# Kernel tuning notes

Hardware: AMD Instinct MI355X
Metric: run time of the kernel (lower is better)

Reference implementation:

```python
import jax, jax.numpy as jnp
import numpy as np

N = 65536
R = 9          # num_relations + 1
D_IN = 256
D_HID = 512
D_OUT = 256
N_HIDDEN = 2


def _xavier(key, shape):
    fan_out, fan_in = shape[-2], shape[-1]
    limit = np.sqrt(6.0 / (fan_in + fan_out))
    return jax.random.uniform(key, shape, jnp.float32, -limit, limit)


def setup_inputs() -> dict:
    key = jax.random.key(0)
    ks = jax.random.split(key, 12)
    inp = {
        "x": jax.random.normal(ks[0], (N, D_IN), jnp.float32),
        "edge_attr": jax.random.uniform(ks[1], (N, R), jnp.float32),
    }
    dims = [(D_HID, D_IN)] + [(D_HID, D_HID)] * N_HIDDEN + [(D_OUT, D_HID)]
    for i, (o, ii) in enumerate(dims):
        inp[f"W{i}"] = _xavier(ks[2 + 2 * i], (R, o, ii))
        inp[f"b{i}"] = _xavier(ks[3 + 2 * i], (R, o))
    return inp


def _linear_kg(x, edge_attr, W, b):
    # roi,ni,nr->no : relation-mixed linear per node
    y = jnp.einsum("roi,ni,nr->no", W, x, edge_attr)
    return y + edge_attr @ b


def reference(x, edge_attr, W0, b0, W1, b1, W2, b2, W3, b3):
    y = jax.nn.relu(_linear_kg(x, edge_attr, W0, b0))
    y = jax.nn.relu(_linear_kg(y, edge_attr, W1, b1))
    y = jax.nn.relu(_linear_kg(y, edge_attr, W2, b2))
    y = _linear_kg(y, edge_attr, W3, b3)
    return y
```

## Files before the change

### kernel.cpp

```cpp
#include <hip/hip_runtime.h>
#include <stdint.h>

using f32x4  = __attribute__((ext_vector_type(4))) float;
using bf16x8 = __attribute__((ext_vector_type(8))) __bf16;

#define GLOAD_LDS16(src, dst) __builtin_amdgcn_global_load_lds(                 \
    (const __attribute__((address_space(1))) void*)(src),                      \
    (__attribute__((address_space(3))) void*)(dst), 16, 0, 0)


__global__ void cvt_x_kernel(const float* __restrict__ x, __bf16* __restrict__ out) {
    const int u    = blockIdx.x * 256 + threadIdx.x;
    const int lane = u & 63;
    const int f    = (u >> 6) & 31;
    const int c    = (u >> 11) & 1;
    const int rb   = u >> 12;
    const int row  = rb * 128 + ((f >> 2) << 4) + (lane & 15);
    const int i    = c * 128 + ((f & 3) << 5) + ((lane >> 4) << 3);
    const float4 a = *(const float4*)(x + (size_t)row * 256 + i);
    const float4 b = *(const float4*)(x + (size_t)row * 256 + i + 4);
    bf16x8 pv;
    pv[0] = (__bf16)a.x; pv[1] = (__bf16)a.y; pv[2] = (__bf16)a.z; pv[3] = (__bf16)a.w;
    pv[4] = (__bf16)b.x; pv[5] = (__bf16)b.y; pv[6] = (__bf16)b.z; pv[7] = (__bf16)b.w;
    *(bf16x8*)(out + (size_t)u * 8) = pv;
}

template<int I, int O>
__global__ void prep_w_kernel(const float* __restrict__ W, __bf16* __restrict__ Bt) {
    constexpr int NCH = I >> 7;
    const int u    = blockIdx.x * 256 + threadIdx.x;
    const int r    = blockIdx.y;
    const int nb   = blockIdx.z;
    const int lane = u & 63;
    const int g    = (u >> 6) & 15;
    const int h    = (u >> 10) & 1;
    const int c    = u >> 11;
    const int mi   = g >> 1;
    const int ks   = (h << 1) + (g & 1);
    const int row  = nb * 128 + mi * 16 + (lane & 15);
    const int i    = c * 128 + ks * 32 + ((lane >> 4) << 3);
    const float* src = W + ((size_t)r * O + row) * I + i;
    const float4 a = *(const float4*)src;
    const float4 b = *(const float4*)(src + 4);
    bf16x8 pv;
    pv[0] = (__bf16)a.x; pv[1] = (__bf16)a.y; pv[2] = (__bf16)a.z; pv[3] = (__bf16)a.w;
    pv[4] = (__bf16)b.x; pv[5] = (__bf16)b.y; pv[6] = (__bf16)b.z; pv[7] = (__bf16)b.w;
    *(bf16x8*)(Bt + ((((size_t)nb * 9 + r) * NCH + c) * 2048 + (u & 2047)) * 8) = pv;
}

template<int O>
__global__ void prep_bias_kernel(const float* __restrict__ b, __bf16* __restrict__ BtB) {
    const int u    = blockIdx.x * 256 + threadIdx.x;
    const int nb   = u >> 10;
    const int q    = u & 1023;
    const int lane = q & 63;
    const int f    = q >> 6;
    const int row  = nb * 128 + ((f >> 1) << 4) + (lane & 15);
    const int kb   = ((f & 1) << 5) + ((lane >> 4) << 3);
    bf16x8 pv;
#pragma unroll
    for (int e = 0; e < 8; ++e) {
        const int k = kb + e;
        pv[e] = (k < 9) ? (__bf16)b[(size_t)k * O + row] : (__bf16)0.f;
    }
    *(bf16x8*)(BtB + (size_t)u * 8) = pv;
}

template<int I, int O, bool RELU, bool OUTF32>
__global__ __launch_bounds__(256, 2)
void kg_gemm(const __bf16* __restrict__ A, const float* __restrict__ E,
             const __bf16* __restrict__ Bt, const __bf16* __restrict__ BtB,
             void* __restrict__ Outv) {
    constexpr int NCH = I >> 7;
    constexpr int NBN = O >> 7;
    static_assert((I & 127) == 0 && (O & 127) == 0, "tile divisibility");

    __shared__ __align__(16) char lds[4 * 16384 + 4608];
    float* const ldsE = (float*)(lds + 65536);

    const int tid  = threadIdx.x;
    const int nwg  = gridDim.x;
    const int braw = blockIdx.x;
    const int bid  = (braw & 7) * (nwg >> 3) + (braw >> 3);
    const int rb   = bid / NBN;
    const int nb   = bid % NBN;
    const int bm0  = rb << 7;
    const int bn0  = nb << 7;
    const int lane = tid & 63;
    const int wid  = tid >> 6;
    const int wr   = (wid >> 1) << 6;
    const int wc   = (wid & 1) << 6;
    const int l15  = lane & 15;
    const int lq   = lane >> 4;

    if (tid < 128) {
        const float* e = E + (size_t)(bm0 + tid) * 9;
#pragma unroll
        for (int q = 0; q < 9; ++q) ldsE[q * 128 + tid] = e[q];
    }
    asm volatile("s_waitcnt lgkmcnt(0)" ::: "memory");

    f32x4 acc[4][4];
#pragma unroll
    for (int m = 0; m < 4; ++m)
#pragma unroll
        for (int n = 0; n < 4; ++n)
            acc[m][n] = f32x4{0.f, 0.f, 0.f, 0.f};
    const f32x4 zero4 = {0.f, 0.f, 0.f, 0.f};

    const size_t Abase = (size_t)rb * NCH * 2048;
    const size_t Bbase = (size_t)nb * 9 * NCH * 2048;
    const int afb = (wr >> 4) << 2;
    const int nfb = (wc >> 4) << 1;

    auto stageS = [&](int s, int c) {
        const __bf16* src = Bt + (Bbase + ((size_t)(s >> 1) * NCH + c) * 2048
                                  + (size_t)((s & 1) << 10)) * 8;
        char* dst = lds + ((s & 3) << 14);
#pragma unroll
        for (int it = 0; it < 4; ++it) {
            const int q = it * 256 + tid;
            GLOAD_LDS16(src + (size_t)q * 8, dst + q * 16);
        }
    };

#pragma unroll 1
    for (int c = 0; c < NCH; ++c) {
        __builtin_amdgcn_s_barrier();
        __builtin_amdgcn_sched_barrier(0);
        bf16x8 af[4][4];
        {
            const __bf16* Ab = A + (Abase + (size_t)c * 2048) * 8;
#pragma unroll
            for (int m = 0; m < 4; ++m)
#pragma unroll
                for (int ks = 0; ks < 4; ++ks)
                    af[m][ks] = *(const bf16x8*)(Ab + ((size_t)((afb + (m << 2) + ks) << 6) + lane) * 8);
        }
        stageS(0, c); stageS(1, c); stageS(2, c); stageS(3, c);

#pragma unroll 1
        for (int r = 0; r < 9; ++r) {
            if (r == 0) asm volatile("s_waitcnt vmcnt(8)" ::: "memory");
            else        asm volatile("s_waitcnt vmcnt(0)" ::: "memory");
            __builtin_amdgcn_s_barrier();
            __builtin_amdgcn_sched_barrier(0);
            if (r >= 1 && r <= 7) { stageS(2 * r + 2, c); stageS(2 * r + 3, c); }

            f32x4 acc2[4][4];
            {
                const char* bp = lds + (((2 * r) & 3) << 14);
                bf16x8 bv[4][2];
#pragma unroll
                for (int n = 0; n < 4; ++n)
#pragma unroll
                    for (int j = 0; j < 2; ++j)
                        bv[n][j] = *(const bf16x8*)(bp + (((nfb + 2 * n + j) << 6) + lane) * 16);
#pragma unroll
                for (int m = 0; m < 4; ++m)
#pragma unroll
                    for (int n = 0; n < 4; ++n) {
                        f32x4 t = __builtin_amdgcn_mfma_f32_16x16x32_bf16(
                            af[m][0], bv[n][0], zero4, 0, 0, 0);
                        acc2[m][n] = __builtin_amdgcn_mfma_f32_16x16x32_bf16(
                            af[m][1], bv[n][1], t, 0, 0, 0);
                    }
            }
            {
                const char* bp = lds + (((2 * r + 1) & 3) << 14);
                bf16x8 bv[4][2];
#pragma unroll
                for (int n = 0; n < 4; ++n)
#pragma unroll
                    for (int j = 0; j < 2; ++j)
                        bv[n][j] = *(const bf16x8*)(bp + (((nfb + 2 * n + j) << 6) + lane) * 16);
#pragma unroll
                for (int m = 0; m < 4; ++m) {
                    const f32x4 evm = *(const f32x4*)(ldsE + r * 128 + wr + m * 16 + lq * 4);
#pragma unroll
                    for (int n = 0; n < 4; ++n) {
                        f32x4 t = __builtin_amdgcn_mfma_f32_16x16x32_bf16(
                            af[m][2], bv[n][0], acc2[m][n], 0, 0, 0);
                        t = __builtin_amdgcn_mfma_f32_16x16x32_bf16(
                            af[m][3], bv[n][1], t, 0, 0, 0);
#pragma unroll
                        for (int j = 0; j < 4; ++j)
                            acc[m][n][j] += evm[j] * t[j];
                    }
                }
            }
        }
    }

    __syncthreads();
    {
        char* const bufB = lds;
        char* const bufA = lds + 16384;
#pragma unroll
        for (int rr = 0; rr < 4; ++rr) {
            const int q = rr * 256 + tid;
            GLOAD_LDS16(BtB + ((size_t)nb * 1024 + q) * 8, bufB + q * 16);
        }
#pragma unroll
        for (int rr = 0; rr < 4; ++rr) {
            const int q    = rr * 256 + tid;
            const int ln   = q & 63;
            const int f    = q >> 6;
            const int row  = ((f >> 1) << 4) + (ln & 15);
            const int kb   = ((f & 1) << 5) + ((ln >> 4) << 3);
            bf16x8 pv;
#pragma unroll
            for (int e8 = 0; e8 < 8; ++e8) {
                const int k = kb + e8;
                pv[e8] = (k < 9) ? (__bf16)ldsE[k * 128 + row] : (__bf16)0.f;
            }
            *(bf16x8*)(bufA + q * 16) = pv;
        }
        __syncthreads();
#pragma unroll
        for (int ks = 0; ks < 2; ++ks) {
            bf16x8 av[4], bv[4];
#pragma unroll
            for (int m = 0; m < 4; ++m)
                av[m] = *(const bf16x8*)(bufA + (((((wr >> 4) + m) * 2 + ks) << 6) + lane) * 16);
#pragma unroll
            for (int n = 0; n < 4; ++n)
                bv[n] = *(const bf16x8*)(bufB + (((((wc >> 4) + n) * 2 + ks) << 6) + lane) * 16);
#pragma unroll
            for (int m = 0; m < 4; ++m)
#pragma unroll
                for (int n = 0; n < 4; ++n)
                    acc[m][n] = __builtin_amdgcn_mfma_f32_16x16x32_bf16(
                        av[m], bv[n], acc[m][n], 0, 0, 0);
        }
    }

    if (OUTF32) {
        const int orow0 = bm0 + wr + lq * 4;
        const int ocol0 = bn0 + wc + l15;
#pragma unroll
        for (int m = 0; m < 4; ++m)
#pragma unroll
            for (int n = 0; n < 4; ++n)
#pragma unroll
                for (int j = 0; j < 4; ++j) {
                    float v = acc[m][n][j];
                    if (RELU) v = fmaxf(v, 0.f);
                    ((float*)Outv)[(size_t)(orow0 + m * 16 + j) * O + (ocol0 + n * 16)] = v;
                }
    } else {
        constexpr int NCHn = O >> 7;
        __bf16* outp = (__bf16*)Outv;
#pragma unroll
        for (int m = 0; m < 4; ++m) {
#pragma unroll
            for (int n = 0; n < 4; ++n) {
                const int col  = bn0 + wc + n * 16 + l15;
                const int c2   = col >> 7;
                const int f2   = (((wr >> 4) + m) << 2) + ((col >> 5) & 3);
                const int ln2  = ((col >> 3) & 3) * 16 + lq * 4;
                const size_t base =
                    (((size_t)rb * NCHn + c2) * 2048 + f2 * 64 + ln2) * 8 + (col & 7);
#pragma unroll
                for (int j = 0; j < 4; ++j) {
                    float v = acc[m][n][j];
                    if (RELU) v = fmaxf(v, 0.f);
                    outp[base + (size_t)j * 8] = (__bf16)v;
                }
            }
        }
    }
}

extern "C" void kernel_launch(void* const* d_in, const int* in_sizes, int n_in,
                              void* d_out, int out_size, void* d_ws, size_t ws_size,
                              hipStream_t stream) {
    const float* x  = (const float*)d_in[0];
    const float* E  = (const float*)d_in[1];
    const float* W0 = (const float*)d_in[2];
    const float* b0 = (const float*)d_in[3];
    const float* W1 = (const float*)d_in[4];
    const float* b1 = (const float*)d_in[5];
    const float* W2 = (const float*)d_in[6];
    const float* b2 = (const float*)d_in[7];
    const float* W3 = (const float*)d_in[8];
    const float* b3 = (const float*)d_in[9];

    char* ws = (char*)d_ws;
    const size_t actBytes = (size_t)65536 * 512 * 2;
    __bf16* actA = (__bf16*)ws;
    __bf16* actB = (__bf16*)(ws + actBytes);
    char* p = ws + 2 * actBytes;
    __bf16* Bt0 = (__bf16*)p; p += (size_t)4 * 9 * 2 * 2048 * 16;
    __bf16* Bt1 = (__bf16*)p; p += (size_t)4 * 9 * 4 * 2048 * 16;
    __bf16* Bt2 = (__bf16*)p; p += (size_t)4 * 9 * 4 * 2048 * 16;
    __bf16* Bt3 = (__bf16*)p; p += (size_t)2 * 9 * 4 * 2048 * 16;
    __bf16* BtB0 = (__bf16*)p; p += (size_t)4 * 1024 * 16;
    __bf16* BtB1 = (__bf16*)p; p += (size_t)4 * 1024 * 16;
    __bf16* BtB2 = (__bf16*)p; p += (size_t)4 * 1024 * 16;
    __bf16* BtB3 = (__bf16*)p; p += (size_t)2 * 1024 * 16;
    if (ws_size < (size_t)(p - ws)) return;

    cvt_x_kernel<<<dim3(8192), dim3(256), 0, stream>>>(x, actA);
    prep_w_kernel<256, 512><<<dim3(16, 9, 4), dim3(256), 0, stream>>>(W0, Bt0);
    prep_w_kernel<512, 512><<<dim3(32, 9, 4), dim3(256), 0, stream>>>(W1, Bt1);
    prep_w_kernel<512, 512><<<dim3(32, 9, 4), dim3(256), 0, stream>>>(W2, Bt2);
    prep_w_kernel<512, 256><<<dim3(32, 9, 2), dim3(256), 0, stream>>>(W3, Bt3);
    prep_bias_kernel<512><<<dim3(16), dim3(256), 0, stream>>>(b0, BtB0);
    prep_bias_kernel<512><<<dim3(16), dim3(256), 0, stream>>>(b1, BtB1);
    prep_bias_kernel<512><<<dim3(16), dim3(256), 0, stream>>>(b2, BtB2);
    prep_bias_kernel<256><<<dim3(8),  dim3(256), 0, stream>>>(b3, BtB3);

    kg_gemm<256, 512, true,  false><<<dim3(2048), dim3(256), 0, stream>>>(actA, E, Bt0, BtB0, actB);
    kg_gemm<512, 512, true,  false><<<dim3(2048), dim3(256), 0, stream>>>(actB, E, Bt1, BtB1, actA);
    kg_gemm<512, 512, true,  false><<<dim3(2048), dim3(256), 0, stream>>>(actA, E, Bt2, BtB2, actB);
    kg_gemm<512, 256, false, true ><<<dim3(1024), dim3(256), 0, stream>>>(actB, E, Bt3, BtB3, d_out);
}
```

Before: 814.6 us.

## Shrink GEMM tile to 64 rows with per-wave private B staging, no barriers

Each workgroup now has two waves covering a 64x128 output tile instead of four waves on 128x128, so twice as many workgroups are launched. Each wave stages its own B slice into a private double-buffered LDS region. The per-relation workgroup barriers are replaced by per-wave vmcnt/lgkmcnt waits, removing cross-wave synchronisation, and LDS use drops so more blocks fit per CU. In exchange, each B tile is now loaded from global once per 64 rows rather than per 128, doubling B traffic. Pipelining within a wave is also shallower.

```diff
diff --git a/kernel.cpp b/kernel.cpp
--- a/kernel.cpp
+++ b/kernel.cpp
@@ -67,7 +67,7 @@
 }
 
 template<int I, int O, bool RELU, bool OUTF32>
-__global__ __launch_bounds__(256, 2)
+__global__ __launch_bounds__(128, 2)
 void kg_gemm(const __bf16* __restrict__ A, const float* __restrict__ E,
              const __bf16* __restrict__ Bt, const __bf16* __restrict__ BtB,
              void* __restrict__ Outv) {
@@ -75,8 +75,8 @@
     constexpr int NBN = O >> 7;
     static_assert((I & 127) == 0 && (O & 127) == 0, "tile divisibility");
 
-    __shared__ __align__(16) char lds[4 * 16384 + 4608];
-    float* const ldsE = (float*)(lds + 65536);
+    __shared__ __align__(16) char lds[32768 + 2816];
+    float* const ldsE = (float*)(lds + 32768);
 
     const int tid  = threadIdx.x;
     const int nwg  = gridDim.x;
@@ -84,21 +84,26 @@
     const int bid  = (braw & 7) * (nwg >> 3) + (braw >> 3);
     const int rb   = bid / NBN;
     const int nb   = bid % NBN;
-    const int bm0  = rb << 7;
+    const int bm0  = rb << 6;
     const int bn0  = nb << 7;
     const int lane = tid & 63;
     const int wid  = tid >> 6;
-    const int wr   = (wid >> 1) << 6;
-    const int wc   = (wid & 1) << 6;
+    const int wc   = wid << 6;
     const int l15  = lane & 15;
     const int lq   = lane >> 4;
-
-    if (tid < 128) {
+    const int afb  = ((bm0 & 127) >> 4) << 2;
+
+    const size_t Abase = (size_t)(bm0 >> 7) * NCH * 2048;
+    const size_t Bbase = (size_t)nb * 9 * NCH * 2048;
+    char* const wlds = lds + (wid << 14);
+
+    if (tid < 64) {
         const float* e = E + (size_t)(bm0 + tid) * 9;
 #pragma unroll
-        for (int q = 0; q < 9; ++q) ldsE[q * 128 + tid] = e[q];
+        for (int q = 0; q < 9; ++q) ldsE[q * 64 + tid] = e[q];
     }
     asm volatile("s_waitcnt lgkmcnt(0)" ::: "memory");
+    __syncthreads();
 
     f32x4 acc[4][4];
 #pragma unroll
@@ -108,25 +113,20 @@
             acc[m][n] = f32x4{0.f, 0.f, 0.f, 0.f};
     const f32x4 zero4 = {0.f, 0.f, 0.f, 0.f};
 
-    const size_t Abase = (size_t)rb * NCH * 2048;
-    const size_t Bbase = (size_t)nb * 9 * NCH * 2048;
-    const int afb = (wr >> 4) << 2;
-    const int nfb = (wc >> 4) << 1;
-
     auto stageS = [&](int s, int c) {
         const __bf16* src = Bt + (Bbase + ((size_t)(s >> 1) * NCH + c) * 2048
-                                  + (size_t)((s & 1) << 10)) * 8;
-        char* dst = lds + ((s & 3) << 14);
-#pragma unroll
-        for (int it = 0; it < 4; ++it) {
-            const int q = it * 256 + tid;
+                                  + ((s & 1) << 10) + (wid << 9)) * 8;
+        char* dst = wlds + ((s & 1) << 13);
+#pragma unroll
+        for (int it = 0; it < 8; ++it) {
+            const int q = it * 64 + lane;
             GLOAD_LDS16(src + (size_t)q * 8, dst + q * 16);
         }
     };
 
 #pragma unroll 1
     for (int c = 0; c < NCH; ++c) {
-        __builtin_amdgcn_s_barrier();
+        asm volatile("s_waitcnt vmcnt(0)" ::: "memory");
         __builtin_amdgcn_sched_barrier(0);
         bf16x8 af[4][4];
         {
@@ -137,73 +137,71 @@
                 for (int ks = 0; ks < 4; ++ks)
                     af[m][ks] = *(const bf16x8*)(Ab + ((size_t)((afb + (m << 2) + ks) << 6) + lane) * 8);
         }
-        stageS(0, c); stageS(1, c); stageS(2, c); stageS(3, c);
+        stageS(0, c); stageS(1, c);
 
 #pragma unroll 1
         for (int r = 0; r < 9; ++r) {
-            if (r == 0) asm volatile("s_waitcnt vmcnt(8)" ::: "memory");
-            else        asm volatile("s_waitcnt vmcnt(0)" ::: "memory");
-            __builtin_amdgcn_s_barrier();
-            __builtin_amdgcn_sched_barrier(0);
-            if (r >= 1 && r <= 7) { stageS(2 * r + 2, c); stageS(2 * r + 3, c); }
-
             f32x4 acc2[4][4];
-            {
-                const char* bp = lds + (((2 * r) & 3) << 14);
+#pragma unroll
+            for (int h = 0; h < 2; ++h) {
+                const int s = 2 * r + h;
+                if (s < 17) asm volatile("s_waitcnt vmcnt(8)" ::: "memory");
+                else        asm volatile("s_waitcnt vmcnt(0)" ::: "memory");
+                __builtin_amdgcn_sched_barrier(0);
+                const char* bp = wlds + ((s & 1) << 13);
                 bf16x8 bv[4][2];
 #pragma unroll
                 for (int n = 0; n < 4; ++n)
 #pragma unroll
                     for (int j = 0; j < 2; ++j)
-                        bv[n][j] = *(const bf16x8*)(bp + (((nfb + 2 * n + j) << 6) + lane) * 16);
-#pragma unroll
-                for (int m = 0; m < 4; ++m)
-#pragma unroll
-                    for (int n = 0; n < 4; ++n) {
-                        f32x4 t = __builtin_amdgcn_mfma_f32_16x16x32_bf16(
-                            af[m][0], bv[n][0], zero4, 0, 0, 0);
-                        acc2[m][n] = __builtin_amdgcn_mfma_f32_16x16x32_bf16(
-                            af[m][1], bv[n][1], t, 0, 0, 0);
-                    }
-            }
-            {
-                const char* bp = lds + (((2 * r + 1) & 3) << 14);
-                bf16x8 bv[4][2];
-#pragma unroll
-                for (int n = 0; n < 4; ++n)
-#pragma unroll
-                    for (int j = 0; j < 2; ++j)
-                        bv[n][j] = *(const bf16x8*)(bp + (((nfb + 2 * n + j) << 6) + lane) * 16);
-#pragma unroll
-                for (int m = 0; m < 4; ++m) {
-                    const f32x4 evm = *(const f32x4*)(ldsE + r * 128 + wr + m * 16 + lq * 4);
-#pragma unroll
-                    for (int n = 0; n < 4; ++n) {
-                        f32x4 t = __builtin_amdgcn_mfma_f32_16x16x32_bf16(
-                            af[m][2], bv[n][0], acc2[m][n], 0, 0, 0);
-                        t = __builtin_amdgcn_mfma_f32_16x16x32_bf16(
-                            af[m][3], bv[n][1], t, 0, 0, 0);
-#pragma unroll
-                        for (int j = 0; j < 4; ++j)
-                            acc[m][n][j] += evm[j] * t[j];
+                        bv[n][j] = *(const bf16x8*)(bp + ((((n << 1) + j) << 6) + lane) * 16);
+                if (h == 0) {
+#pragma unroll
+                    for (int m = 0; m < 4; ++m)
+#pragma unroll
+                        for (int n = 0; n < 4; ++n) {
+                            f32x4 t = __builtin_amdgcn_mfma_f32_16x16x32_bf16(
+                                af[m][0], bv[n][0], zero4, 0, 0, 0);
+                            acc2[m][n] = __builtin_amdgcn_mfma_f32_16x16x32_bf16(
+                                af[m][1], bv[n][1], t, 0, 0, 0);
+                        }
+                } else {
+#pragma unroll
+                    for (int m = 0; m < 4; ++m) {
+                        const f32x4 evm = *(const f32x4*)(ldsE + r * 64 + m * 16 + lq * 4);
+#pragma unroll
+                        for (int n = 0; n < 4; ++n) {
+                            f32x4 t = __builtin_amdgcn_mfma_f32_16x16x32_bf16(
+                                af[m][2], bv[n][0], acc2[m][n], 0, 0, 0);
+                            t = __builtin_amdgcn_mfma_f32_16x16x32_bf16(
+                                af[m][3], bv[n][1], t, 0, 0, 0);
+#pragma unroll
+                            for (int j = 0; j < 4; ++j)
+                                acc[m][n][j] += evm[j] * t[j];
+                        }
                     }
                 }
+                if (s + 2 <= 17) {
+                    asm volatile("s_waitcnt lgkmcnt(0)" ::: "memory");
+                    __builtin_amdgcn_sched_barrier(0);
+                    stageS(s + 2, c);
+                }
             }
         }
     }
 
     __syncthreads();
     {
-        char* const bufB = lds;
-        char* const bufA = lds + 16384;
-#pragma unroll
-        for (int rr = 0; rr < 4; ++rr) {
-            const int q = rr * 256 + tid;
-            GLOAD_LDS16(BtB + ((size_t)nb * 1024 + q) * 8, bufB + q * 16);
-        }
-#pragma unroll
-        for (int rr = 0; rr < 4; ++rr) {
-            const int q    = rr * 256 + tid;
+        const __bf16* srcB = BtB + ((size_t)nb * 1024 + (wid << 9)) * 8;
+#pragma unroll
+        for (int it = 0; it < 8; ++it) {
+            const int q = it * 64 + lane;
+            GLOAD_LDS16(srcB + (size_t)q * 8, wlds + q * 16);
+        }
+        char* const bufA = lds + 8192;
+#pragma unroll
+        for (int it = 0; it < 4; ++it) {
+            const int q    = it * 128 + tid;
             const int ln   = q & 63;
             const int f    = q >> 6;
             const int row  = ((f >> 1) << 4) + (ln & 15);
@@ -212,7 +210,7 @@
 #pragma unroll
             for (int e8 = 0; e8 < 8; ++e8) {
                 const int k = kb + e8;
-                pv[e8] = (k < 9) ? (__bf16)ldsE[k * 128 + row] : (__bf16)0.f;
+                pv[e8] = (k < 9) ? (__bf16)ldsE[k * 64 + row] : (__bf16)0.f;
             }
             *(bf16x8*)(bufA + q * 16) = pv;
         }
@@ -222,10 +220,10 @@
             bf16x8 av[4], bv[4];
 #pragma unroll
             for (int m = 0; m < 4; ++m)
-                av[m] = *(const bf16x8*)(bufA + (((((wr >> 4) + m) * 2 + ks) << 6) + lane) * 16);
+                av[m] = *(const bf16x8*)(bufA + ((((m << 1) + ks) << 6) + lane) * 16);
 #pragma unroll
             for (int n = 0; n < 4; ++n)
-                bv[n] = *(const bf16x8*)(bufB + (((((wc >> 4) + n) * 2 + ks) << 6) + lane) * 16);
+                bv[n] = *(const bf16x8*)(wlds + ((((n << 1) + ks) << 6) + lane) * 16);
 #pragma unroll
             for (int m = 0; m < 4; ++m)
 #pragma unroll
@@ -236,7 +234,7 @@
     }
 
     if (OUTF32) {
-        const int orow0 = bm0 + wr + lq * 4;
+        const int orow0 = bm0 + lq * 4;
         const int ocol0 = bn0 + wc + l15;
 #pragma unroll
         for (int m = 0; m < 4; ++m)
@@ -251,16 +249,18 @@
     } else {
         constexpr int NCHn = O >> 7;
         __bf16* outp = (__bf16*)Outv;
+        const int mib = (bm0 & 127) >> 4;
+        const int rbo = bm0 >> 7;
 #pragma unroll
         for (int m = 0; m < 4; ++m) {
 #pragma unroll
             for (int n = 0; n < 4; ++n) {
                 const int col  = bn0 + wc + n * 16 + l15;
                 const int c2   = col >> 7;
-                const int f2   = (((wr >> 4) + m) << 2) + ((col >> 5) & 3);
+                const int f2   = ((mib + m) << 2) + ((col >> 5) & 3);
                 const int ln2  = ((col >> 3) & 3) * 16 + lq * 4;
                 const size_t base =
-                    (((size_t)rb * NCHn + c2) * 2048 + f2 * 64 + ln2) * 8 + (col & 7);
+                    (((size_t)rbo * NCHn + c2) * 2048 + f2 * 64 + ln2) * 8 + (col & 7);
 #pragma unroll
                 for (int j = 0; j < 4; ++j) {
                     float v = acc[m][n][j];
@@ -311,8 +311,8 @@
     prep_bias_kernel<512><<<dim3(16), dim3(256), 0, stream>>>(b2, BtB2);
     prep_bias_kernel<256><<<dim3(8),  dim3(256), 0, stream>>>(b3, BtB3);
 
-    kg_gemm<256, 512, true,  false><<<dim3(2048), dim3(256), 0, stream>>>(actA, E, Bt0, BtB0, actB);
-    kg_gemm<512, 512, true,  false><<<dim3(2048), dim3(256), 0, stream>>>(actB, E, Bt1, BtB1, actA);
-    kg_gemm<512, 512, true,  false><<<dim3(2048), dim3(256), 0, stream>>>(actA, E, Bt2, BtB2, actB);
-    kg_gemm<512, 256, false, true ><<<dim3(1024), dim3(256), 0, stream>>>(actB, E, Bt3, BtB3, d_out);
-}
+    kg_gemm<256, 512, true,  false><<<dim3(4096), dim3(128), 0, stream>>>(actA, E, Bt0, BtB0, actB);
+    kg_gemm<512, 512, true,  false><<<dim3(4096), dim3(128), 0, stream>>>(actB, E, Bt1, BtB1, actA);
+    kg_gemm<512, 512, true,  false><<<dim3(4096), dim3(128), 0, stream>>>(actA, E, Bt2, BtB2, actB);
+    kg_gemm<512, 256, false, true ><<<dim3(2048), dim3(128), 0, stream>>>(actB, E, Bt3, BtB3, d_out);
+}
```

Measured after the change: 1.008 ms. +23.7%, slower.
